# Kernel optimization log

Hardware: AMD Instinct MI355X
Metric: run time of the kernel (lower is better)

Reference implementation:

```python
import jax, jax.numpy as jnp
import numpy as np
import math

PHI = (1.0 + math.sqrt(5.0)) / 2.0
LUT_SIZE = 4096
D_MODEL = 2048
BATCH = 8192
TWO_PI = 2.0 * math.pi


def lut_sin_cos(theta, sin_table, cos_table):
    """LUT-based sin/cos with linear interpolation over [0, 2*pi)."""
    n = sin_table.shape[0]
    pos = jnp.mod(theta, TWO_PI) * (n / TWO_PI)        # [B, D] in [0, n)
    i0f = jnp.floor(pos)
    frac = pos - i0f
    i0 = i0f.astype(jnp.int32) % n
    i1 = (i0 + 1) % n
    s = sin_table[i0] * (1.0 - frac) + sin_table[i1] * frac
    c = cos_table[i0] * (1.0 - frac) + cos_table[i1] * frac
    return s, c


def setup_inputs() -> dict:
    key = jax.random.key(0)
    ks = jax.random.split(key, 6)
    x_real = jax.random.normal(ks[0], (BATCH, D_MODEL), dtype=jnp.float32)
    x_imag = jax.random.normal(ks[1], (BATCH, D_MODEL), dtype=jnp.float32)
    t = jax.random.uniform(ks[2], (BATCH,), dtype=jnp.float32)
    memory_real = jnp.zeros((BATCH, D_MODEL), dtype=jnp.float32)
    memory_imag = jnp.zeros((BATCH, D_MODEL), dtype=jnp.float32)
    w_trigger = jax.random.normal(ks[3], (D_MODEL,), dtype=jnp.float32) * 0.02
    b_trigger = jnp.zeros((D_MODEL,), dtype=jnp.float32)
    w_state = jax.random.normal(ks[4], (D_MODEL,), dtype=jnp.float32) * 0.02
    b_state = jnp.zeros((D_MODEL,), dtype=jnp.float32)
    k = jnp.asarray(3.0, dtype=jnp.float32)
    grid = jnp.arange(LUT_SIZE, dtype=jnp.float32) * (TWO_PI / LUT_SIZE)
    sin_table = jnp.sin(grid)
    cos_table = jnp.cos(grid)
    return dict(x_real=x_real, x_imag=x_imag, t=t,
                memory_real=memory_real, memory_imag=memory_imag,
                w_trigger=w_trigger, b_trigger=b_trigger,
                w_state=w_state, b_state=b_state, k=k,
                sin_table=sin_table, cos_table=cos_table)


def reference(x_real, x_imag, t, memory_real, memory_imag,
              w_trigger, b_trigger, w_state, b_state, k,
              sin_table, cos_table):
    scale = math.sqrt(x_real.shape[-1])
    t_phi = t[:, None] * PHI                                  # [B, 1]

    # trigger phase
    wl_trigger = 1.0 + jnp.abs(w_trigger)
    theta_tr = x_real / wl_trigger + b_trigger + t_phi
    theta_ti = x_imag / wl_trigger + b_trigger + t_phi
    sin_tr, cos_tr = lut_sin_cos(theta_tr, sin_table, cos_table)
    sin_ti, cos_ti = lut_sin_cos(theta_ti, sin_table, cos_table)
    trigger_real = cos_tr * cos_ti - sin_tr * sin_ti
    trigger_imag = cos_tr * sin_ti + sin_tr * cos_ti

    # interference -> exponential decay gate
    interference_raw = jnp.sum(trigger_real * x_real + trigger_imag * x_imag, axis=-1)
    interference_clamped = jnp.clip(interference_raw / scale, -1.0, 1.0)
    x_inv = (1.0 - interference_clamped) / 2.0
    k_eff = jnp.abs(k) + 0.1
    alpha = jnp.exp(-k_eff * x_inv)[:, None]                  # [B, 1]

    # blend with (detached) memory, then re-evolve
    blended_real = alpha * x_real + (1.0 - alpha) * memory_real
    blended_imag = alpha * x_imag + (1.0 - alpha) * memory_imag
    wl_state = 1.0 + jnp.abs(w_state)
    theta_sr = blended_real / wl_state + b_state + t_phi
    theta_si = blended_imag / wl_state + b_state + t_phi
    sin_sr, cos_sr = lut_sin_cos(theta_sr, sin_table, cos_table)
    sin_si, cos_si = lut_sin_cos(theta_si, sin_table, cos_table)
    evolved_real = cos_sr * cos_si - sin_sr * sin_si
    evolved_imag = cos_sr * sin_si + sin_sr * cos_si
    return evolved_real, evolved_imag
```

## Files before the change

kernel.cpp:

```cpp
#include <hip/hip_runtime.h>

#define DMODEL   2048
#define NTHREADS 256

__device__ __forceinline__ void fast_sincos(float theta, float& s, float& c) {
    const float INV_TWO_PI = 0.15915494309189535f;
    float r  = theta * INV_TWO_PI;
    float rr = r - floorf(r);
#if __has_builtin(__builtin_amdgcn_sinf) && __has_builtin(__builtin_amdgcn_cosf)
    s = __builtin_amdgcn_sinf(rr);
    c = __builtin_amdgcn_cosf(rr);
#else
    s = __sinf(rr * 6.283185307179586f);
    c = __cosf(rr * 6.283185307179586f);
#endif
}

__device__ __forceinline__ float fast_rcp(float x) {
#if __has_builtin(__builtin_amdgcn_rcpf)
    return __builtin_amdgcn_rcpf(x);
#else
    return 1.0f / x;
#endif
}

__global__ __launch_bounds__(NTHREADS)
void liquid_echo_kernel(const float* __restrict__ x_real,
                        const float* __restrict__ x_imag,
                        const float* __restrict__ tvec,
                        const float* __restrict__ memory_real,
                        const float* __restrict__ memory_imag,
                        const float* __restrict__ w_trigger,
                        const float* __restrict__ b_trigger,
                        const float* __restrict__ w_state,
                        const float* __restrict__ b_state,
                        const float* __restrict__ kptr,
                        float* __restrict__ out,
                        size_t imag_off)
{
    __shared__ float red[NTHREADS / 64];

    const int tid = threadIdx.x;
    const int row = blockIdx.x;

    const float t_phi = tvec[row] * 1.6180339887498948f;
    const int c0 = tid * 4;
    const int c1 = (DMODEL / 2) + tid * 4;
    const size_t rb = (size_t)row * DMODEL;

    float4 xr0 = *(const float4*)(x_real + rb + c0);
    float4 xr1 = *(const float4*)(x_real + rb + c1);
    float4 xi0 = *(const float4*)(x_imag + rb + c0);
    float4 xi1 = *(const float4*)(x_imag + rb + c1);
    float4 wt0 = *(const float4*)(w_trigger + c0);
    float4 wt1 = *(const float4*)(w_trigger + c1);
    float4 bt0 = *(const float4*)(b_trigger + c0);
    float4 bt1 = *(const float4*)(b_trigger + c1);

    float xrv[8] = {xr0.x, xr0.y, xr0.z, xr0.w, xr1.x, xr1.y, xr1.z, xr1.w};
    float xiv[8] = {xi0.x, xi0.y, xi0.z, xi0.w, xi1.x, xi1.y, xi1.z, xi1.w};
    float wtv[8] = {wt0.x, wt0.y, wt0.z, wt0.w, wt1.x, wt1.y, wt1.z, wt1.w};
    float btv[8] = {bt0.x, bt0.y, bt0.z, bt0.w, bt1.x, bt1.y, bt1.z, bt1.w};

    float sxy[8];
    float partial = 0.0f;
    #pragma unroll
    for (int j = 0; j < 8; ++j) {
        float iw   = fast_rcp(1.0f + fabsf(wtv[j]));
        float base = btv[j] + t_phi;
        sxy[j]     = xrv[j] + xiv[j];
        float ths  = fmaf(sxy[j], iw, base + base);
        float s, c;
        fast_sincos(ths, s, c);
        partial = fmaf(c, xrv[j], partial);
        partial = fmaf(s, xiv[j], partial);
    }

    float4 mr0 = *(const float4*)(memory_real + rb + c0);
    float4 mr1 = *(const float4*)(memory_real + rb + c1);
    float4 mi0 = *(const float4*)(memory_imag + rb + c0);
    float4 mi1 = *(const float4*)(memory_imag + rb + c1);
    float4 ws0 = *(const float4*)(w_state + c0);
    float4 ws1 = *(const float4*)(w_state + c1);
    float4 bs0 = *(const float4*)(b_state + c0);
    float4 bs1 = *(const float4*)(b_state + c1);

    #pragma unroll
    for (int off = 32; off > 0; off >>= 1)
        partial += __shfl_down(partial, off, 64);
    if ((tid & 63) == 0) red[tid >> 6] = partial;
    __syncthreads();

    float tot   = red[0] + red[1] + red[2] + red[3];
    float ic    = tot * (1.0f / 45.254833995939045f);
    ic          = fminf(1.0f, fmaxf(-1.0f, ic));
    float x_inv = (1.0f - ic) * 0.5f;
    float k_eff = fabsf(kptr[0]) + 0.1f;
    const float alpha = __expf(-k_eff * x_inv);
    const float oma   = 1.0f - alpha;

    float mrv[8] = {mr0.x, mr0.y, mr0.z, mr0.w, mr1.x, mr1.y, mr1.z, mr1.w};
    float miv[8] = {mi0.x, mi0.y, mi0.z, mi0.w, mi1.x, mi1.y, mi1.z, mi1.w};
    float wsv[8] = {ws0.x, ws0.y, ws0.z, ws0.w, ws1.x, ws1.y, ws1.z, ws1.w};
    float bsv[8] = {bs0.x, bs0.y, bs0.z, bs0.w, bs1.x, bs1.y, bs1.z, bs1.w};

    float er[8], ei[8];
    #pragma unroll
    for (int j = 0; j < 8; ++j) {
        float sb   = fmaf(alpha, sxy[j], oma * (mrv[j] + miv[j]));
        float iw   = fast_rcp(1.0f + fabsf(wsv[j]));
        float base = bsv[j] + t_phi;
        float ths  = fmaf(sb, iw, base + base);
        float s, c;
        fast_sincos(ths, s, c);
        er[j] = c;
        ei[j] = s;
    }

    float* outr = out + rb;
    float* outi = out + imag_off + rb;
    *(float4*)(outr + c0) = make_float4(er[0], er[1], er[2], er[3]);
    *(float4*)(outr + c1) = make_float4(er[4], er[5], er[6], er[7]);
    *(float4*)(outi + c0) = make_float4(ei[0], ei[1], ei[2], ei[3]);
    *(float4*)(outi + c1) = make_float4(ei[4], ei[5], ei[6], ei[7]);
}

extern "C" void kernel_launch(void* const* d_in, const int* in_sizes, int n_in,
                              void* d_out, int out_size, void* d_ws, size_t ws_size,
                              hipStream_t stream) {
    const float* x_real      = (const float*)d_in[0];
    const float* x_imag      = (const float*)d_in[1];
    const float* t           = (const float*)d_in[2];
    const float* memory_real = (const float*)d_in[3];
    const float* memory_imag = (const float*)d_in[4];
    const float* w_trigger   = (const float*)d_in[5];
    const float* b_trigger   = (const float*)d_in[6];
    const float* w_state     = (const float*)d_in[7];
    const float* b_state     = (const float*)d_in[8];
    const float* k           = (const float*)d_in[9];
    float* out = (float*)d_out;

    int B = in_sizes[0] / DMODEL;
    size_t imag_off = (size_t)out_size / 2;

    liquid_echo_kernel<<<B, NTHREADS, 0, stream>>>(
        x_real, x_imag, t, memory_real, memory_imag,
        w_trigger, b_trigger, w_state, b_state, k,
        out, imag_off);
}
```

Measured before the change: 330.9 us.

## Use persistent grid-stride rows with hoisted weight reciprocals and nontemporal stores

The kernel now launches a fixed grid of 2048 blocks, each looping over several rows, instead of one block per row. The weight and bias loads and the reciprocal of (1+|w|) are computed once per block and reused across rows. All memory loads for a row are issued up front, and outputs are written with nontemporal stores. The goal is less per-block setup and better cache behaviour in a memory-bound kernel, at the cost of an extra __syncthreads per row and fewer resident blocks to hide latency.

```diff
diff --git a/kernel.cpp b/kernel.cpp
--- a/kernel.cpp
+++ b/kernel.cpp
@@ -2,6 +2,9 @@
 
 #define DMODEL   2048
 #define NTHREADS 256
+#define NBLOCKS  2048
+
+typedef float f32x4 __attribute__((ext_vector_type(4)));
 
 __device__ __forceinline__ void fast_sincos(float theta, float& s, float& c) {
     const float INV_TWO_PI = 0.15915494309189535f;
@@ -36,93 +39,105 @@
                         const float* __restrict__ b_state,
                         const float* __restrict__ kptr,
                         float* __restrict__ out,
-                        size_t imag_off)
+                        size_t imag_off, int nrows)
 {
     __shared__ float red[NTHREADS / 64];
 
     const int tid = threadIdx.x;
-    const int row = blockIdx.x;
+    const int c0  = tid * 4;
+    const int c1  = (DMODEL / 2) + tid * 4;
 
-    const float t_phi = tvec[row] * 1.6180339887498948f;
-    const int c0 = tid * 4;
-    const int c1 = (DMODEL / 2) + tid * 4;
-    const size_t rb = (size_t)row * DMODEL;
-
-    float4 xr0 = *(const float4*)(x_real + rb + c0);
-    float4 xr1 = *(const float4*)(x_real + rb + c1);
-    float4 xi0 = *(const float4*)(x_imag + rb + c0);
-    float4 xi1 = *(const float4*)(x_imag + rb + c1);
     float4 wt0 = *(const float4*)(w_trigger + c0);
     float4 wt1 = *(const float4*)(w_trigger + c1);
     float4 bt0 = *(const float4*)(b_trigger + c0);
     float4 bt1 = *(const float4*)(b_trigger + c1);
-
-    float xrv[8] = {xr0.x, xr0.y, xr0.z, xr0.w, xr1.x, xr1.y, xr1.z, xr1.w};
-    float xiv[8] = {xi0.x, xi0.y, xi0.z, xi0.w, xi1.x, xi1.y, xi1.z, xi1.w};
-    float wtv[8] = {wt0.x, wt0.y, wt0.z, wt0.w, wt1.x, wt1.y, wt1.z, wt1.w};
-    float btv[8] = {bt0.x, bt0.y, bt0.z, bt0.w, bt1.x, bt1.y, bt1.z, bt1.w};
-
-    float sxy[8];
-    float partial = 0.0f;
-    #pragma unroll
-    for (int j = 0; j < 8; ++j) {
-        float iw   = fast_rcp(1.0f + fabsf(wtv[j]));
-        float base = btv[j] + t_phi;
-        sxy[j]     = xrv[j] + xiv[j];
-        float ths  = fmaf(sxy[j], iw, base + base);
-        float s, c;
-        fast_sincos(ths, s, c);
-        partial = fmaf(c, xrv[j], partial);
-        partial = fmaf(s, xiv[j], partial);
-    }
-
-    float4 mr0 = *(const float4*)(memory_real + rb + c0);
-    float4 mr1 = *(const float4*)(memory_real + rb + c1);
-    float4 mi0 = *(const float4*)(memory_imag + rb + c0);
-    float4 mi1 = *(const float4*)(memory_imag + rb + c1);
     float4 ws0 = *(const float4*)(w_state + c0);
     float4 ws1 = *(const float4*)(w_state + c1);
     float4 bs0 = *(const float4*)(b_state + c0);
     float4 bs1 = *(const float4*)(b_state + c1);
 
-    #pragma unroll
-    for (int off = 32; off > 0; off >>= 1)
-        partial += __shfl_down(partial, off, 64);
-    if ((tid & 63) == 0) red[tid >> 6] = partial;
-    __syncthreads();
-
-    float tot   = red[0] + red[1] + red[2] + red[3];
-    float ic    = tot * (1.0f / 45.254833995939045f);
-    ic          = fminf(1.0f, fmaxf(-1.0f, ic));
-    float x_inv = (1.0f - ic) * 0.5f;
-    float k_eff = fabsf(kptr[0]) + 0.1f;
-    const float alpha = __expf(-k_eff * x_inv);
-    const float oma   = 1.0f - alpha;
-
-    float mrv[8] = {mr0.x, mr0.y, mr0.z, mr0.w, mr1.x, mr1.y, mr1.z, mr1.w};
-    float miv[8] = {mi0.x, mi0.y, mi0.z, mi0.w, mi1.x, mi1.y, mi1.z, mi1.w};
-    float wsv[8] = {ws0.x, ws0.y, ws0.z, ws0.w, ws1.x, ws1.y, ws1.z, ws1.w};
+    float iwt[8] = {fast_rcp(1.0f + fabsf(wt0.x)), fast_rcp(1.0f + fabsf(wt0.y)),
+                    fast_rcp(1.0f + fabsf(wt0.z)), fast_rcp(1.0f + fabsf(wt0.w)),
+                    fast_rcp(1.0f + fabsf(wt1.x)), fast_rcp(1.0f + fabsf(wt1.y)),
+                    fast_rcp(1.0f + fabsf(wt1.z)), fast_rcp(1.0f + fabsf(wt1.w))};
+    float btv[8] = {bt0.x, bt0.y, bt0.z, bt0.w, bt1.x, bt1.y, bt1.z, bt1.w};
+    float iws[8] = {fast_rcp(1.0f + fabsf(ws0.x)), fast_rcp(1.0f + fabsf(ws0.y)),
+                    fast_rcp(1.0f + fabsf(ws0.z)), fast_rcp(1.0f + fabsf(ws0.w)),
+                    fast_rcp(1.0f + fabsf(ws1.x)), fast_rcp(1.0f + fabsf(ws1.y)),
+                    fast_rcp(1.0f + fabsf(ws1.z)), fast_rcp(1.0f + fabsf(ws1.w))};
     float bsv[8] = {bs0.x, bs0.y, bs0.z, bs0.w, bs1.x, bs1.y, bs1.z, bs1.w};
 
-    float er[8], ei[8];
-    #pragma unroll
-    for (int j = 0; j < 8; ++j) {
-        float sb   = fmaf(alpha, sxy[j], oma * (mrv[j] + miv[j]));
-        float iw   = fast_rcp(1.0f + fabsf(wsv[j]));
-        float base = bsv[j] + t_phi;
-        float ths  = fmaf(sb, iw, base + base);
-        float s, c;
-        fast_sincos(ths, s, c);
-        er[j] = c;
-        ei[j] = s;
+    const float k_eff = fabsf(kptr[0]) + 0.1f;
+
+    #pragma unroll 1
+    for (int row = blockIdx.x; row < nrows; row += NBLOCKS) {
+        const size_t rb = (size_t)row * DMODEL;
+        const float t_phi = tvec[row] * 1.6180339887498948f;
+
+        float4 xr0 = *(const float4*)(x_real + rb + c0);
+        float4 xr1 = *(const float4*)(x_real + rb + c1);
+        float4 xi0 = *(const float4*)(x_imag + rb + c0);
+        float4 xi1 = *(const float4*)(x_imag + rb + c1);
+        float4 mr0 = *(const float4*)(memory_real + rb + c0);
+        float4 mr1 = *(const float4*)(memory_real + rb + c1);
+        float4 mi0 = *(const float4*)(memory_imag + rb + c0);
+        float4 mi1 = *(const float4*)(memory_imag + rb + c1);
+
+        float xrv[8] = {xr0.x, xr0.y, xr0.z, xr0.w, xr1.x, xr1.y, xr1.z, xr1.w};
+        float xiv[8] = {xi0.x, xi0.y, xi0.z, xi0.w, xi1.x, xi1.y, xi1.z, xi1.w};
+
+        float sxy[8];
+        float partial = 0.0f;
+        #pragma unroll
+        for (int j = 0; j < 8; ++j) {
+            float base = btv[j] + t_phi;
+            sxy[j]     = xrv[j] + xiv[j];
+            float ths  = fmaf(sxy[j], iwt[j], base + base);
+            float s, c;
+            fast_sincos(ths, s, c);
+            partial = fmaf(c, xrv[j], partial);
+            partial = fmaf(s, xiv[j], partial);
+        }
+
+        #pragma unroll
+        for (int off = 32; off > 0; off >>= 1)
+            partial += __shfl_down(partial, off, 64);
+        __syncthreads();
+        if ((tid & 63) == 0) red[tid >> 6] = partial;
+        __syncthreads();
+
+        float tot   = red[0] + red[1] + red[2] + red[3];
+        float ic    = tot * (1.0f / 45.254833995939045f);
+        ic          = fminf(1.0f, fmaxf(-1.0f, ic));
+        float x_inv = (1.0f - ic) * 0.5f;
+        const float alpha = __expf(-k_eff * x_inv);
+        const float oma   = 1.0f - alpha;
+
+        float mrv[8] = {mr0.x, mr0.y, mr0.z, mr0.w, mr1.x, mr1.y, mr1.z, mr1.w};
+        float miv[8] = {mi0.x, mi0.y, mi0.z, mi0.w, mi1.x, mi1.y, mi1.z, mi1.w};
+
+        float er[8], ei[8];
+        #pragma unroll
+        for (int j = 0; j < 8; ++j) {
+            float sb  = fmaf(alpha, sxy[j], oma * (mrv[j] + miv[j]));
+            float ths = fmaf(sb, iws[j], (bsv[j] + t_phi) * 2.0f);
+            float s, c;
+            fast_sincos(ths, s, c);
+            er[j] = c;
+            ei[j] = s;
+        }
+
+        float* outr = out + rb;
+        float* outi = out + imag_off + rb;
+        f32x4 vr0 = {er[0], er[1], er[2], er[3]};
+        f32x4 vr1 = {er[4], er[5], er[6], er[7]};
+        f32x4 vi0 = {ei[0], ei[1], ei[2], ei[3]};
+        f32x4 vi1 = {ei[4], ei[5], ei[6], ei[7]};
+        __builtin_nontemporal_store(vr0, (f32x4*)(outr + c0));
+        __builtin_nontemporal_store(vr1, (f32x4*)(outr + c1));
+        __builtin_nontemporal_store(vi0, (f32x4*)(outi + c0));
+        __builtin_nontemporal_store(vi1, (f32x4*)(outi + c1));
     }
-
-    float* outr = out + rb;
-    float* outi = out + imag_off + rb;
-    *(float4*)(outr + c0) = make_float4(er[0], er[1], er[2], er[3]);
-    *(float4*)(outr + c1) = make_float4(er[4], er[5], er[6], er[7]);
-    *(float4*)(outi + c0) = make_float4(ei[0], ei[1], ei[2], ei[3]);
-    *(float4*)(outi + c1) = make_float4(ei[4], ei[5], ei[6], ei[7]);
 }
 
 extern "C" void kernel_launch(void* const* d_in, const int* in_sizes, int n_in,
@@ -142,9 +157,10 @@
 
     int B = in_sizes[0] / DMODEL;
     size_t imag_off = (size_t)out_size / 2;
+    int grid = (B < NBLOCKS) ? B : NBLOCKS;
 
-    liquid_echo_kernel<<<B, NTHREADS, 0, stream>>>(
+    liquid_echo_kernel<<<grid, NTHREADS, 0, stream>>>(
         x_real, x_imag, t, memory_real, memory_imag,
         w_trigger, b_trigger, w_state, b_state, k,
-        out, imag_off);
+        out, imag_off, B);
 }
```

Measured after the change: 342.9 us. 1.04x slower.
